# Kernel tuning notes

Measured on AMD Instinct MI355X. Metric: run time of the kernel, lower is better.

The kernel has to match this reference:

```python
import jax, jax.numpy as jnp
import numpy as np

K_TOP = 2  # top-k experts per token


def setup_inputs() -> dict:
    key = jax.random.key(0)
    k1, k2, k3 = jax.random.split(key, 3)
    B, S, H, E = 4, 2048, 1024, 8
    hidden_states = jax.random.normal(k1, (B, S, H), dtype=jnp.float32)
    router_w = jax.random.normal(k2, (E, H), dtype=jnp.float32) * 0.02
    expert_weights = jax.random.normal(k3, (E, H, H), dtype=jnp.float32) * 0.02
    return {"hidden_states": hidden_states, "router_w": router_w, "expert_weights": expert_weights}


def reference(hidden_states, router_w, expert_weights):
    B, S, H = hidden_states.shape
    x = hidden_states.reshape(-1, H)                      # [N, H], N = B*S
    logits = x @ router_w.T                               # [N, E]
    probs = jax.nn.softmax(logits, axis=-1)               # [N, E]
    topk_vals, topk_idx = jax.lax.top_k(probs, K_TOP)     # [N, K]
    topk_w = topk_vals / (topk_vals.sum(-1, keepdims=True) + 1e-6)  # [N, K]

    # Dense per-expert GEMM over all tokens (single-device dispatch = identity)
    expert_out = jnp.einsum('nh,eho->eno', x, expert_weights)  # [E, N, H]

    # all_to_all_combine: gather each token's K expert outputs
    combined = jnp.take_along_axis(
        expert_out.transpose(1, 0, 2),                    # [N, E, H]
        topk_idx[:, :, None], axis=1)                     # [N, K, H]
    combined = combined.transpose(1, 0, 2)                # [K, N, H]

    # remap bias: sum over last dim of one-hot(topk_idx) * router_prob == gathered prob
    remap_bias = jnp.take_along_axis(probs, topk_idx, axis=1).T[:, :, None]  # [K, N, 1]

    weights = topk_w.T[:, :, None]                        # [K, N, 1]
    out = ((combined + remap_bias) * weights).sum(axis=0) # [N, H]
    return out.reshape(B, S, H)
```

## Files before the change

kernel.cpp:

```cpp
#include <hip/hip_runtime.h>
#include <hip/hip_fp16.h>
#include <cstdint>

typedef unsigned short u16;
typedef __attribute__((ext_vector_type(8))) short short8;
typedef __attribute__((ext_vector_type(4))) float float4v;

#define NTOK 8192
#define HDIM 1024
#define NEXP 8
#define TM 256
#define TN 256
#define BK 64
#define KTILES (HDIM / BK)
#define NIT (KTILES / 2)
#define HTILE (128 * 64)
#define MAXT 72
#define WBLK 8192
#define RBLK 2048

__device__ __forceinline__ u16 f2bf(float f) {
    union { float f; uint32_t u; } v; v.f = f;
    uint32_t u = v.u;
    return (u16)((u + 0x7FFFu + ((u >> 16) & 1u)) >> 16);
}

__device__ __forceinline__ void gll16(const u16* g, u16* l) {
    __builtin_amdgcn_global_load_lds(
        (const __attribute__((address_space(1))) uint32_t*)g,
        (__attribute__((address_space(3))) uint32_t*)l,
        16, 0, 0);
}

__global__ __launch_bounds__(256) void prep(const float* __restrict__ x,
                                            const float* __restrict__ rw,
                                            const float* __restrict__ ew,
                                            u16* __restrict__ x_bf,
                                            u16* __restrict__ w_bf,
                                            float* __restrict__ wt0,
                                            float* __restrict__ wt1,
                                            float* __restrict__ biasv,
                                            int* __restrict__ sel,
                                            int* __restrict__ ctrl) {
    if (blockIdx.x == 0 && threadIdx.x < 132) ctrl[threadIdx.x] = 0;

    if (blockIdx.x < WBLK) {
        __shared__ float tile[32][33];
        const int bid = blockIdx.x;
        const int e  = bid >> 10;
        const int k0 = (bid & 31) * 32;
        const int n0 = ((bid >> 5) & 31) * 32;
        const int r = threadIdx.x >> 3;
        const int c = (threadIdx.x & 7) * 4;
        const float4 v = *(const float4*)(ew + ((size_t)e << 20) + (size_t)(k0 + r) * HDIM + n0 + c);
        tile[r][c] = v.x; tile[r][c+1] = v.y; tile[r][c+2] = v.z; tile[r][c+3] = v.w;
        __syncthreads();
        ushort4 o;
        o.x = f2bf(tile[c][r]); o.y = f2bf(tile[c+1][r]);
        o.z = f2bf(tile[c+2][r]); o.w = f2bf(tile[c+3][r]);
        *(ushort4*)(w_bf + ((size_t)e << 20) + (size_t)(n0 + r) * HDIM + k0 + c) = o;
    } else {
        const int wv = threadIdx.x >> 6;
        const int l  = threadIdx.x & 63;
        const int n  = (blockIdx.x - WBLK) * 4 + wv;
        const float4* xr = (const float4*)(x + (size_t)n * HDIM);
        ushort4* xo = (ushort4*)(x_bf + (size_t)n * HDIM);

        float4 xv[4];
#pragma unroll
        for (int t = 0; t < 4; t++) {
            xv[t] = xr[t * 64 + l];
            ushort4 p;
            p.x = f2bf(xv[t].x); p.y = f2bf(xv[t].y);
            p.z = f2bf(xv[t].z); p.w = f2bf(xv[t].w);
            xo[t * 64 + l] = p;
        }

        float logits[NEXP];
#pragma unroll
        for (int e = 0; e < NEXP; e++) {
            const float4* rwe = (const float4*)(rw + e * HDIM);
            float acc = 0.f;
#pragma unroll
            for (int t = 0; t < 4; t++) {
                const float4 r = rwe[t * 64 + l];
                acc += xv[t].x * r.x + xv[t].y * r.y + xv[t].z * r.z + xv[t].w * r.w;
            }
#pragma unroll
            for (int s = 32; s > 0; s >>= 1) acc += __shfl_xor(acc, s, 64);
            logits[e] = acc;
        }

        if (l == 0) {
            float mx = logits[0];
#pragma unroll
            for (int e = 1; e < NEXP; e++) mx = fmaxf(mx, logits[e]);
            float p[NEXP]; float sum = 0.f;
#pragma unroll
            for (int e = 0; e < NEXP; e++) { p[e] = expf(logits[e] - mx); sum += p[e]; }
            const float inv = 1.f / sum;
#pragma unroll
            for (int e = 0; e < NEXP; e++) p[e] *= inv;
            int e0 = 0;
#pragma unroll
            for (int e = 1; e < NEXP; e++) if (p[e] > p[e0]) e0 = e;
            int e1 = (e0 == 0) ? 1 : 0;
#pragma unroll
            for (int e = 0; e < NEXP; e++) if (e != e0 && p[e] > p[e1]) e1 = e;
            const float p0 = p[e0], p1 = p[e1];
            const float wsum = p0 + p1 + 1e-6f;
            const float w0 = p0 / wsum, w1 = p1 / wsum;
            wt0[n] = w0; wt1[n] = w1;
            biasv[n] = w0 * p0 + w1 * p1;
            sel[n] = e0 | (e1 << 8);
        }
    }
}

__global__ __launch_bounds__(256) void build_lists(const int* __restrict__ sel,
                                                   int* __restrict__ lists,
                                                   int* __restrict__ ctrl,
                                                   int* __restrict__ tmap) {
    const int n  = blockIdx.x * 256 + threadIdx.x;
    const int wv = threadIdx.x >> 6;
    const int l  = threadIdx.x & 63;
    const int s  = sel[n];
    const int e0 = s & 0xFF, e1 = s >> 8;
    __shared__ int wcnt[NEXP][4];
    __shared__ int ebase[NEXP];
    int pf0 = 0, pf1 = 0;
    const unsigned long long ltmask = (1ULL << l) - 1ULL;
#pragma unroll
    for (int e = 0; e < NEXP; e++) {
        const int slot = (e0 == e) ? 0 : ((e1 == e) ? 1 : -1);
        const unsigned long long bal = __ballot(slot >= 0);
        const int pf = __popcll(bal & ltmask);
        if (slot == 0) pf0 = pf;
        if (slot == 1) pf1 = pf;
        if (l == 0) wcnt[e][wv] = __popcll(bal);
    }
    __syncthreads();
    if (threadIdx.x < NEXP) {
        const int e = threadIdx.x;
        const int tot = wcnt[e][0] + wcnt[e][1] + wcnt[e][2] + wcnt[e][3];
        ebase[e] = atomicAdd(&ctrl[e * 16], tot);
    }
    __syncthreads();
    int off0 = ebase[e0], off1 = ebase[e1];
#pragma unroll
    for (int i = 0; i < 4; i++) {
        off0 += (i < wv) ? wcnt[e0][i] : 0;
        off1 += (i < wv) ? wcnt[e1][i] : 0;
    }
    lists[e0 * NTOK + off0 + pf0] = n;
    lists[e1 * NTOK + off1 + pf1] = n | 0x10000;

    __shared__ int lastflag;
    __threadfence();
    if (threadIdx.x == 0) lastflag = (atomicAdd(&ctrl[128], 1) == (int)gridDim.x - 1);
    __syncthreads();
    if (lastflag) {
        __shared__ int tbase[NEXP + 1];
        if (threadIdx.x == 0) {
            int acc = 0;
            for (int e = 0; e < NEXP; e++) {
                tbase[e] = acc;
                acc += (atomicAdd(&ctrl[e * 16], 0) + TM - 1) / TM;
            }
            tbase[NEXP] = acc;
        }
        __syncthreads();
        for (int i = threadIdx.x; i < MAXT; i += 256) {
            int v = -1;
#pragma unroll
            for (int e = 0; e < NEXP; e++)
                if (i >= tbase[e] && i < tbase[e + 1]) v = (e << 16) | (i - tbase[e]);
            tmap[i] = v;
        }
    }
}

__global__ __launch_bounds__(512, 2) void moe_gemm(const u16* __restrict__ x_bf,
                                                   const u16* __restrict__ wt_bf,
                                                   const int* __restrict__ lists,
                                                   const int* __restrict__ ctrl,
                                                   const int* __restrict__ tmap,
                                                   const float* __restrict__ wt0,
                                                   const float* __restrict__ wt1,
                                                   const float* __restrict__ biasv,
                                                   __half* __restrict__ stage0,
                                                   __half* __restrict__ stage1) {
    const int ent = tmap[blockIdx.x];
    if (ent < 0) return;
    const int e = ent >> 16;
    const int tile_m = (ent & 0xFFFF) * TM;
    const int cnt = ctrl[e * 16];
    const int tn = blockIdx.y * TN;

    __shared__ u16 lA[4 * HTILE];
    __shared__ u16 lB[4 * HTILE];
    __shared__ int   toks[TM];
    __shared__ float wgt[TM];
    __shared__ float bia[TM];
    __shared__ int   slt[TM];

    const int t  = threadIdx.x;
    const int wv = t >> 6;
    const int l  = t & 63;

    if (t < TM) {
        const int idx = tile_m + t;
        int tok = 0; float w = 0.f, b = 0.f; int sl = 0;
        if (idx < cnt) {
            const int entry = lists[e * NTOK + idx];
            tok = entry & 0xFFFF;
            sl = entry >> 16;
            w = sl ? wt1[tok] : wt0[tok];
            b = sl ? 0.f : biasv[tok];
        }
        toks[t] = tok; wgt[t] = w; bia[t] = b; slt[t] = sl;
    }
    __syncthreads();

    const u16* const wbase = wt_bf + ((size_t)e << 20);
    const u16* pA[2][2]; const u16* pB[2][2];
    int dst0, dst1;
    {
        const int s0 = (0 * 8 + wv) * 64 + l;
        const int s1 = (1 * 8 + wv) * 64 + l;
        const int r0 = s0 >> 3, r1 = s1 >> 3;
        const int g0s = (s0 & 7) ^ (r0 & 7);
        const int g1s = (s1 & 7) ^ (r1 & 7);
        dst0 = (0 * 8 + wv) * 512;
        dst1 = (1 * 8 + wv) * 512;
#pragma unroll
        for (int h = 0; h < 2; h++) {
            pA[0][h] = x_bf + (size_t)toks[h * 128 + r0] * HDIM + g0s * 8;
            pA[1][h] = x_bf + (size_t)toks[h * 128 + r1] * HDIM + g1s * 8;
            pB[0][h] = wbase + (size_t)(tn + h * 128 + r0) * HDIM + g0s * 8;
            pB[1][h] = wbase + (size_t)(tn + h * 128 + r1) * HDIM + g1s * 8;
        }
    }

#define STAGE_A(par, h, ktile) do { \
    gll16(pA[0][h] + (ktile) * 64, lA + (par) * 2 * HTILE + (h) * HTILE + dst0); \
    gll16(pA[1][h] + (ktile) * 64, lA + (par) * 2 * HTILE + (h) * HTILE + dst1); } while (0)
#define STAGE_B(par, h, ktile) do { \
    gll16(pB[0][h] + (ktile) * 64, lB + (par) * 2 * HTILE + (h) * HTILE + dst0); \
    gll16(pB[1][h] + (ktile) * 64, lB + (par) * 2 * HTILE + (h) * HTILE + dst1); } while (0)

    const int wm2 = wv >> 2;
    const int wn4 = wv & 3;
    const int fm = l & 15;
    const int fq = l >> 4;
    const int f7 = fm & 7;
    const int pg0 = ((0 + fq) ^ f7) * 8;
    const int pg1 = ((4 + fq) ^ f7) * 8;
    const int arow = fm * 64;
    const int brow = (wn4 & 1) * 4096 + fm * 64;
    const u16* const Abase = lA + wm2 * HTILE;
    const u16* const Bbase = lB + (wn4 >> 1) * HTILE;

    short8 afr[4][2];
    short8 bfr[2][2][2];

#define LDA_H(par, mq) do { \
    _Pragma("unroll") \
    for (int mfL = 0; mfL < 4; mfL++) { \
        afr[mfL][0] = *(const short8*)(Abase + (par) * 2 * HTILE + ((mq) * 4 + mfL) * 1024 + arow + pg0); \
        afr[mfL][1] = *(const short8*)(Abase + (par) * 2 * HTILE + ((mq) * 4 + mfL) * 1024 + arow + pg1); \
    } } while (0)
#define LDB_H(par, nq) do { \
    _Pragma("unroll") \
    for (int nfL = 0; nfL < 2; nfL++) { \
        bfr[nq][nfL][0] = *(const short8*)(Bbase + (par) * 2 * HTILE + ((nq) * 2 + nfL) * 1024 + brow + pg0); \
        bfr[nq][nfL][1] = *(const short8*)(Bbase + (par) * 2 * HTILE + ((nq) * 2 + nfL) * 1024 + brow + pg1); \
    } } while (0)

    float4v acc[8][4];
#pragma unroll
    for (int i = 0; i < 8; i++)
#pragma unroll
        for (int j = 0; j < 4; j++) { float4v z = {0.f, 0.f, 0.f, 0.f}; acc[i][j] = z; }

#define MFMA_Q(mq, nq) do { \
    __builtin_amdgcn_s_setprio(1); \
    _Pragma("unroll") \
    for (int ks = 0; ks < 2; ks++) \
    _Pragma("unroll") \
    for (int mfL = 0; mfL < 4; mfL++) \
    _Pragma("unroll") \
    for (int nfL = 0; nfL < 2; nfL++) \
        acc[(mq) * 4 + mfL][(nq) * 2 + nfL] = __builtin_amdgcn_mfma_f32_16x16x32_bf16( \
            afr[mfL][ks], bfr[nq][nfL][ks], acc[(mq) * 4 + mfL][(nq) * 2 + nfL], 0, 0, 0); \
    __builtin_amdgcn_s_setprio(0); } while (0)

#define BARx() __builtin_amdgcn_s_barrier()
#define LGKM0 do { asm volatile("s_waitcnt lgkmcnt(0)" ::: "memory"); \
                   __builtin_amdgcn_sched_barrier(0); } while (0)
#define VM2 asm volatile("s_waitcnt vmcnt(2)" ::: "memory")
#define VM0 asm volatile("s_waitcnt vmcnt(0)" ::: "memory")

    STAGE_A(0, 0, 0); STAGE_A(0, 1, 0);
    STAGE_B(0, 0, 0); STAGE_B(0, 1, 0);
    STAGE_A(1, 0, 1);
    VM0; BARx();

#pragma unroll
    for (int it = 0; it < NIT; ++it) {
        const bool st = (it < NIT - 1);
        LDA_H(0, 0); LDB_H(0, 0);
        STAGE_A(1, 1, 2 * it + 1);
        BARx(); LGKM0;
        MFMA_Q(0, 0);
        BARx();
        LDB_H(0, 1);
        STAGE_B(1, 0, 2 * it + 1);
        BARx(); LGKM0;
        MFMA_Q(0, 1);
        BARx();
        LDA_H(0, 1);
        STAGE_B(1, 1, 2 * it + 1);
        BARx(); LGKM0;
        MFMA_Q(1, 1);
        BARx();
        if (st) STAGE_A(0, 0, 2 * it + 2);
        BARx();
        MFMA_Q(1, 0);
        if (st) { VM2; } else { VM0; }
        BARx();
        LDA_H(1, 0); LDB_H(1, 0);
        if (st) STAGE_A(0, 1, 2 * it + 2);
        BARx(); LGKM0;
        MFMA_Q(0, 0);
        BARx();
        LDB_H(1, 1);
        if (st) STAGE_B(0, 0, 2 * it + 2);
        BARx(); LGKM0;
        MFMA_Q(0, 1);
        BARx();
        LDA_H(1, 1);
        if (st) STAGE_B(0, 1, 2 * it + 2);
        BARx(); LGKM0;
        MFMA_Q(1, 1);
        BARx();
        if (st) STAGE_A(1, 0, 2 * it + 3);
        BARx();
        MFMA_Q(1, 0);
        if (st) { VM2; } else { VM0; }
        BARx();
    }

#pragma unroll
    for (int mf = 0; mf < 8; mf++) {
#pragma unroll
        for (int r = 0; r < 4; r++) {
            const int m_local = wm2 * 128 + mf * 16 + fq * 4 + r;
            if (tile_m + m_local < cnt) {
                const int tok = toks[m_local];
                const float w = wgt[m_local], b = bia[m_local];
                __half* sp = (slt[m_local] ? stage1 : stage0) + (size_t)tok * HDIM;
#pragma unroll
                for (int nf = 0; nf < 4; nf++) {
                    const int h = tn + wn4 * 64 + nf * 16 + fm;
                    sp[h] = __float2half(acc[mf][nf][r] * w + b);
                }
            }
        }
    }
#undef STAGE_A
#undef STAGE_B
#undef LDA_H
#undef LDB_H
#undef MFMA_Q
#undef BARx
#undef LGKM0
#undef VM2
#undef VM0
}

__global__ __launch_bounds__(256) void combine(const __half* __restrict__ s0,
                                               const __half* __restrict__ s1,
                                               float* __restrict__ out) {
    const size_t idx = ((size_t)blockIdx.x * 256 + threadIdx.x) * 8;
    union { uint4 v; __half h[8]; } a, b;
    a.v = *(const uint4*)(s0 + idx);
    b.v = *(const uint4*)(s1 + idx);
    float4 o0, o1;
    o0.x = __half2float(a.h[0]) + __half2float(b.h[0]);
    o0.y = __half2float(a.h[1]) + __half2float(b.h[1]);
    o0.z = __half2float(a.h[2]) + __half2float(b.h[2]);
    o0.w = __half2float(a.h[3]) + __half2float(b.h[3]);
    o1.x = __half2float(a.h[4]) + __half2float(b.h[4]);
    o1.y = __half2float(a.h[5]) + __half2float(b.h[5]);
    o1.z = __half2float(a.h[6]) + __half2float(b.h[6]);
    o1.w = __half2float(a.h[7]) + __half2float(b.h[7]);
    *(float4*)(out + idx)     = o0;
    *(float4*)(out + idx + 4) = o1;
}

extern "C" void kernel_launch(void* const* d_in, const int* in_sizes, int n_in,
                              void* d_out, int out_size, void* d_ws, size_t ws_size,
                              hipStream_t stream) {
    const float* x  = (const float*)d_in[0];
    const float* rw = (const float*)d_in[1];
    const float* ew = (const float*)d_in[2];
    float* out = (float*)d_out;

    char* ws = (char*)d_ws;
    u16*    x_bf   = (u16*)ws;
    u16*    w_bf   = (u16*)(ws + 16777216);
    __half* stage0 = (__half*)(ws + 33554432);
    __half* stage1 = (__half*)(ws + 50331648);
    float*  wt0    = (float*)(ws + 67108864);
    float*  wt1    = (float*)(ws + 67141632);
    float*  biasv  = (float*)(ws + 67174400);
    int*    sel    = (int*)(ws + 67207168);
    int*    lists  = (int*)(ws + 67239936);
    int*    ctrl   = (int*)(ws + 67502080);
    int*    tmap   = (int*)(ws + 67502720);

    prep<<<WBLK + RBLK, 256, 0, stream>>>(x, rw, ew, x_bf, w_bf, wt0, wt1, biasv, sel, ctrl);
    build_lists<<<NTOK / 256, 256, 0, stream>>>(sel, lists, ctrl, tmap);
    moe_gemm<<<dim3(MAXT, HDIM / TN, 1), 512, 0, stream>>>(
        x_bf, w_bf, lists, ctrl, tmap, wt0, wt1, biasv, stage0, stage1);
    combine<<<(NTOK * HDIM) / (256 * 8), 256, 0, stream>>>(stage0, stage1, out);
}
```

Measured before the change: 203.8 us.

## Split MoE GEMM into fat 256-tile and thin 128-tile kernels for tail tiles

The grouped expert GEMM now runs as two launches. The first 64 tiles of 256 tokens go to the existing 256x256 kernel. The remaining tail tiles are split into 128x128 tiles handled by a new 256-thread kernel with a three-stage LDS pipeline, which spreads the ragged tail work over more blocks and reduces wave-quantization idle time on the device. The weight transpose/convert prep also moves to 64x64 tiles with fewer, larger blocks. The cost is an extra kernel launch and a second tile map, plus the risk that the thin kernel is less efficient per FLOP.

New measurement: 198.2 us. 1.03x faster.

```diff
diff --git a/kernel.cpp b/kernel.cpp
--- a/kernel.cpp
+++ b/kernel.cpp
@@ -9,14 +9,15 @@
 #define NTOK 8192
 #define HDIM 1024
 #define NEXP 8
-#define TM 256
-#define TN 256
-#define BK 64
-#define KTILES (HDIM / BK)
-#define NIT (KTILES / 2)
 #define HTILE (128 * 64)
-#define MAXT 72
-#define WBLK 8192
+#define NITF 8
+#define MAXT256 72
+#define FATT 64
+#define TMT 128
+#define BKT 32
+#define NITT (HDIM / BKT)
+#define LAT (TMT * BKT)
+#define WBLK 2048
 #define RBLK 2048
 
 __device__ __forceinline__ u16 f2bf(float f) {
@@ -45,20 +46,35 @@
     if (blockIdx.x == 0 && threadIdx.x < 132) ctrl[threadIdx.x] = 0;
 
     if (blockIdx.x < WBLK) {
-        __shared__ float tile[32][33];
+        __shared__ float tile[64][65];
         const int bid = blockIdx.x;
-        const int e  = bid >> 10;
-        const int k0 = (bid & 31) * 32;
-        const int n0 = ((bid >> 5) & 31) * 32;
-        const int r = threadIdx.x >> 3;
-        const int c = (threadIdx.x & 7) * 4;
-        const float4 v = *(const float4*)(ew + ((size_t)e << 20) + (size_t)(k0 + r) * HDIM + n0 + c);
-        tile[r][c] = v.x; tile[r][c+1] = v.y; tile[r][c+2] = v.z; tile[r][c+3] = v.w;
+        const int e  = bid >> 8;
+        const int k0 = ((bid >> 4) & 15) * 64;
+        const int n0 = (bid & 15) * 64;
+        const int kr = threadIdx.x >> 2;
+        const int ng = (threadIdx.x & 3) * 16;
+        const float* src = ew + ((size_t)e << 20) + (size_t)(k0 + kr) * HDIM + n0 + ng;
+#pragma unroll
+        for (int j = 0; j < 4; j++) {
+            const float4 v = *(const float4*)(src + 4 * j);
+            tile[kr][ng + 4*j]     = v.x;
+            tile[kr][ng + 4*j + 1] = v.y;
+            tile[kr][ng + 4*j + 2] = v.z;
+            tile[kr][ng + 4*j + 3] = v.w;
+        }
         __syncthreads();
-        ushort4 o;
-        o.x = f2bf(tile[c][r]); o.y = f2bf(tile[c+1][r]);
-        o.z = f2bf(tile[c+2][r]); o.w = f2bf(tile[c+3][r]);
-        *(ushort4*)(w_bf + ((size_t)e << 20) + (size_t)(n0 + r) * HDIM + k0 + c) = o;
+        const int nr = threadIdx.x >> 2;
+        const int kg = (threadIdx.x & 3) * 16;
+        u16* dst = w_bf + ((size_t)e << 20) + (size_t)(n0 + nr) * HDIM + k0 + kg;
+#pragma unroll
+        for (int j = 0; j < 4; j++) {
+            ushort4 o;
+            o.x = f2bf(tile[kg + 4*j][nr]);
+            o.y = f2bf(tile[kg + 4*j + 1][nr]);
+            o.z = f2bf(tile[kg + 4*j + 2][nr]);
+            o.w = f2bf(tile[kg + 4*j + 3][nr]);
+            *(ushort4*)(dst + 4 * j) = o;
+        }
     } else {
         const int wv = threadIdx.x >> 6;
         const int l  = threadIdx.x & 63;
@@ -120,7 +136,8 @@
 __global__ __launch_bounds__(256) void build_lists(const int* __restrict__ sel,
                                                    int* __restrict__ lists,
                                                    int* __restrict__ ctrl,
-                                                   int* __restrict__ tmap) {
+                                                   int* __restrict__ tmap,
+                                                   int* __restrict__ tmap128) {
     const int n  = blockIdx.x * 256 + threadIdx.x;
     const int wv = threadIdx.x >> 6;
     const int l  = threadIdx.x & 63;
@@ -161,54 +178,71 @@
     __syncthreads();
     if (lastflag) {
         __shared__ int tbase[NEXP + 1];
+        __shared__ int cnts[NEXP];
         if (threadIdx.x == 0) {
             int acc = 0;
             for (int e = 0; e < NEXP; e++) {
                 tbase[e] = acc;
-                acc += (atomicAdd(&ctrl[e * 16], 0) + TM - 1) / TM;
+                cnts[e] = atomicAdd(&ctrl[e * 16], 0);
+                acc += (cnts[e] + 255) / 256;
             }
             tbase[NEXP] = acc;
         }
         __syncthreads();
-        for (int i = threadIdx.x; i < MAXT; i += 256) {
+        for (int i = threadIdx.x; i < MAXT256; i += 256) {
             int v = -1;
 #pragma unroll
             for (int e = 0; e < NEXP; e++)
                 if (i >= tbase[e] && i < tbase[e + 1]) v = (e << 16) | (i - tbase[e]);
             tmap[i] = v;
         }
-    }
-}
-
-__global__ __launch_bounds__(512, 2) void moe_gemm(const u16* __restrict__ x_bf,
-                                                   const u16* __restrict__ wt_bf,
-                                                   const int* __restrict__ lists,
-                                                   const int* __restrict__ ctrl,
-                                                   const int* __restrict__ tmap,
-                                                   const float* __restrict__ wt0,
-                                                   const float* __restrict__ wt1,
-                                                   const float* __restrict__ biasv,
-                                                   __half* __restrict__ stage0,
-                                                   __half* __restrict__ stage1) {
+        if (threadIdx.x < 16) {
+            const int j = threadIdx.x;
+            const int i256 = FATT + (j >> 1);
+            int v = -1;
+            if (i256 < tbase[NEXP]) {
+                int ve = 0;
+#pragma unroll
+                for (int e = 0; e < NEXP; e++)
+                    if (i256 >= tbase[e] && i256 < tbase[e + 1]) ve = e;
+                const int m256 = i256 - tbase[ve];
+                const int m128 = m256 * 2 + (j & 1);
+                if (m128 * 128 < cnts[ve]) v = (ve << 16) | m128;
+            }
+            tmap128[j] = v;
+        }
+    }
+}
+
+__global__ __launch_bounds__(512, 2) void moe_gemm_fat(const u16* __restrict__ x_bf,
+                                                       const u16* __restrict__ wt_bf,
+                                                       const int* __restrict__ lists,
+                                                       const int* __restrict__ ctrl,
+                                                       const int* __restrict__ tmap,
+                                                       const float* __restrict__ wt0,
+                                                       const float* __restrict__ wt1,
+                                                       const float* __restrict__ biasv,
+                                                       __half* __restrict__ stage0,
+                                                       __half* __restrict__ stage1) {
     const int ent = tmap[blockIdx.x];
     if (ent < 0) return;
     const int e = ent >> 16;
-    const int tile_m = (ent & 0xFFFF) * TM;
+    const int tile_m = (ent & 0xFFFF) * 256;
     const int cnt = ctrl[e * 16];
-    const int tn = blockIdx.y * TN;
+    const int tn = blockIdx.y * 256;
 
     __shared__ u16 lA[4 * HTILE];
     __shared__ u16 lB[4 * HTILE];
-    __shared__ int   toks[TM];
-    __shared__ float wgt[TM];
-    __shared__ float bia[TM];
-    __shared__ int   slt[TM];
+    __shared__ int   toks[256];
+    __shared__ float wgt[256];
+    __shared__ float bia[256];
+    __shared__ int   slt[256];
 
     const int t  = threadIdx.x;
     const int wv = t >> 6;
     const int l  = t & 63;
 
-    if (t < TM) {
+    if (t < 256) {
         const int idx = tile_m + t;
         int tok = 0; float w = 0.f, b = 0.f; int sl = 0;
         if (idx < cnt) {
@@ -307,8 +341,8 @@
     VM0; BARx();
 
 #pragma unroll
-    for (int it = 0; it < NIT; ++it) {
-        const bool st = (it < NIT - 1);
+    for (int it = 0; it < NITF; ++it) {
+        const bool st = (it < NITF - 1);
         LDA_H(0, 0); LDB_H(0, 0);
         STAGE_A(1, 1, 2 * it + 1);
         BARx(); LGKM0;
@@ -377,6 +411,159 @@
 #undef LGKM0
 #undef VM2
 #undef VM0
+}
+
+__global__ __launch_bounds__(256, 3) void moe_gemm_thin(const u16* __restrict__ x_bf,
+                                                        const u16* __restrict__ wt_bf,
+                                                        const int* __restrict__ lists,
+                                                        const int* __restrict__ ctrl,
+                                                        const int* __restrict__ tmap128,
+                                                        const float* __restrict__ wt0,
+                                                        const float* __restrict__ wt1,
+                                                        const float* __restrict__ biasv,
+                                                        __half* __restrict__ stage0,
+                                                        __half* __restrict__ stage1) {
+    const int ent = tmap128[blockIdx.x];
+    if (ent < 0) return;
+    const int e = ent >> 16;
+    const int tile_m = (ent & 0xFFFF) * TMT;
+    const int cnt = ctrl[e * 16];
+    const int tn = blockIdx.y * TMT;
+
+    __shared__ u16 lA[3 * LAT];
+    __shared__ u16 lB[3 * LAT];
+    __shared__ int   toks[TMT];
+    __shared__ float wgt[TMT];
+    __shared__ float bia[TMT];
+    __shared__ int   slt[TMT];
+
+    const int t  = threadIdx.x;
+    const int wv = t >> 6;
+    const int l  = t & 63;
+
+    if (t < TMT) {
+        const int idx = tile_m + t;
+        int tok = 0; float w = 0.f, b = 0.f; int sl = 0;
+        if (idx < cnt) {
+            const int entry = lists[e * NTOK + idx];
+            tok = entry & 0xFFFF;
+            sl = entry >> 16;
+            w = sl ? wt1[tok] : wt0[tok];
+            b = sl ? 0.f : biasv[tok];
+        }
+        toks[t] = tok; wgt[t] = w; bia[t] = b; slt[t] = sl;
+    }
+    __syncthreads();
+
+    const u16* gA[2]; const u16* gB[2]; int dAB[2];
+#pragma unroll
+    for (int i = 0; i < 2; i++) {
+        const int slot = (i * 4 + wv) * 64 + l;
+        const int row  = slot >> 2;
+        const int c    = (slot & 3) ^ ((row >> 1) & 3);
+        gA[i] = x_bf + (size_t)toks[row] * HDIM + c * 8;
+        gB[i] = wt_bf + ((size_t)e << 20) + (size_t)(tn + row) * HDIM + c * 8;
+        dAB[i] = (i * 4 + wv) * 512;
+    }
+
+    const int wm = (wv & 1) * 64;
+    const int wn = (wv >> 1) * 64;
+    const int fm = l & 15;
+    const int fq = l >> 4;
+    int aoff[4], boff[4];
+#pragma unroll
+    for (int i = 0; i < 4; i++) {
+        const int ra = wm + i * 16 + fm;
+        const int rb = wn + i * 16 + fm;
+        aoff[i] = ra * BKT + ((fq ^ ((ra >> 1) & 3)) * 8);
+        boff[i] = rb * BKT + ((fq ^ ((rb >> 1) & 3)) * 8);
+    }
+
+    float4v acc[4][4];
+#pragma unroll
+    for (int i = 0; i < 4; i++)
+#pragma unroll
+        for (int j = 0; j < 4; j++) { float4v z = {0.f, 0.f, 0.f, 0.f}; acc[i][j] = z; }
+
+    short8 afr[2][4], bfr[2][4];
+
+#pragma unroll
+    for (int tk = 0; tk < 3; tk++) {
+#pragma unroll
+        for (int i = 0; i < 2; i++) {
+            gll16(gA[i] + tk * BKT, lA + tk * LAT + dAB[i]);
+            gll16(gB[i] + tk * BKT, lB + tk * LAT + dAB[i]);
+        }
+    }
+    asm volatile("s_waitcnt vmcnt(8)\n\ts_barrier" ::: "memory");
+#pragma unroll
+    for (int i = 0; i < 4; i++) {
+        afr[0][i] = *(const short8*)&lA[aoff[i]];
+        bfr[0][i] = *(const short8*)&lB[boff[i]];
+    }
+
+#pragma unroll
+    for (int it = 0; it < NITT; ++it) {
+        const int cs = it & 1;
+        const int ns = cs ^ 1;
+
+        if (it == 0) {
+            asm volatile("s_waitcnt vmcnt(4)\n\ts_barrier" ::: "memory");
+        } else if (it < NITT - 1) {
+            asm volatile("s_waitcnt vmcnt(0)\n\ts_barrier" ::: "memory");
+        }
+
+        if (it >= 1 && it + 2 < NITT) {
+            const int nb = (it + 2) % 3;
+            const int nk = (it + 2) * BKT;
+#pragma unroll
+            for (int i = 0; i < 2; i++) {
+                gll16(gA[i] + nk, lA + nb * LAT + dAB[i]);
+                gll16(gB[i] + nk, lB + nb * LAT + dAB[i]);
+            }
+        }
+
+        if (it + 1 < NITT) {
+            const u16* ca = lA + ((it + 1) % 3) * LAT;
+            const u16* cb = lB + ((it + 1) % 3) * LAT;
+#pragma unroll
+            for (int i = 0; i < 4; i++) {
+                afr[ns][i] = *(const short8*)&ca[aoff[i]];
+                bfr[ns][i] = *(const short8*)&cb[boff[i]];
+            }
+            asm volatile("s_waitcnt lgkmcnt(8)" ::: "memory");
+        } else {
+            asm volatile("s_waitcnt lgkmcnt(0)" ::: "memory");
+        }
+        __builtin_amdgcn_sched_barrier(0);
+
+        __builtin_amdgcn_s_setprio(1);
+#pragma unroll
+        for (int i = 0; i < 4; i++)
+#pragma unroll
+            for (int nf = 0; nf < 4; nf++)
+                acc[i][nf] = __builtin_amdgcn_mfma_f32_16x16x32_bf16(
+                    afr[cs][i], bfr[cs][nf], acc[i][nf], 0, 0, 0);
+        __builtin_amdgcn_s_setprio(0);
+    }
+
+#pragma unroll
+    for (int mf = 0; mf < 4; mf++) {
+#pragma unroll
+        for (int r = 0; r < 4; r++) {
+            const int m_local = wm + mf * 16 + fq * 4 + r;
+            if (tile_m + m_local < cnt) {
+                const int tok = toks[m_local];
+                const float w = wgt[m_local], b = bia[m_local];
+                __half* sp = (slt[m_local] ? stage1 : stage0) + (size_t)tok * HDIM;
+#pragma unroll
+                for (int nf = 0; nf < 4; nf++) {
+                    const int h = tn + wn + nf * 16 + fm;
+                    sp[h] = __float2half(acc[mf][nf][r] * w + b);
+                }
+            }
+        }
+    }
 }
 
 __global__ __launch_bounds__(256) void combine(const __half* __restrict__ s0,
@@ -408,21 +595,24 @@
     float* out = (float*)d_out;
 
     char* ws = (char*)d_ws;
-    u16*    x_bf   = (u16*)ws;
-    u16*    w_bf   = (u16*)(ws + 16777216);
-    __half* stage0 = (__half*)(ws + 33554432);
-    __half* stage1 = (__half*)(ws + 50331648);
-    float*  wt0    = (float*)(ws + 67108864);
-    float*  wt1    = (float*)(ws + 67141632);
-    float*  biasv  = (float*)(ws + 67174400);
-    int*    sel    = (int*)(ws + 67207168);
-    int*    lists  = (int*)(ws + 67239936);
-    int*    ctrl   = (int*)(ws + 67502080);
-    int*    tmap   = (int*)(ws + 67502720);
+    u16*    x_bf    = (u16*)ws;
+    u16*    w_bf    = (u16*)(ws + 16777216);
+    __half* stage0  = (__half*)(ws + 33554432);
+    __half* stage1  = (__half*)(ws + 50331648);
+    float*  wt0     = (float*)(ws + 67108864);
+    float*  wt1     = (float*)(ws + 67141632);
+    float*  biasv   = (float*)(ws + 67174400);
+    int*    sel     = (int*)(ws + 67207168);
+    int*    lists   = (int*)(ws + 67239936);
+    int*    ctrl    = (int*)(ws + 67502080);
+    int*    tmap    = (int*)(ws + 67502720);
+    int*    tmap128 = (int*)(ws + 67503104);
 
     prep<<<WBLK + RBLK, 256, 0, stream>>>(x, rw, ew, x_bf, w_bf, wt0, wt1, biasv, sel, ctrl);
-    build_lists<<<NTOK / 256, 256, 0, stream>>>(sel, lists, ctrl, tmap);
-    moe_gemm<<<dim3(MAXT, HDIM / TN, 1), 512, 0, stream>>>(
+    build_lists<<<NTOK / 256, 256, 0, stream>>>(sel, lists, ctrl, tmap, tmap128);
+    moe_gemm_fat<<<dim3(FATT, 4, 1), 512, 0, stream>>>(
         x_bf, w_bf, lists, ctrl, tmap, wt0, wt1, biasv, stage0, stage1);
+    moe_gemm_thin<<<dim3(16, 8, 1), 256, 0, stream>>>(
+        x_bf, w_bf, lists, ctrl, tmap128, wt0, wt1, biasv, stage0, stage1);
     combine<<<(NTOK * HDIM) / (256 * 8), 256, 0, stream>>>(stage0, stage1, out);
 }
```
